# Kernel tuning notes

Measured on AMD Instinct MI355X. Metric: run time of the kernel, lower is better.

## Reference

```python
import jax, jax.numpy as jnp
import numpy as np

D_MODEL = 1024


def setup_inputs() -> dict:
    key = jax.random.key(0)
    k_x, k_qkv, k_proj, k_b = jax.random.split(key, 4)
    b, t, d = 4, 2048, D_MODEL
    scale = 1.0 / np.sqrt(d)
    x = jax.random.normal(k_x, (b, t, d), dtype=jnp.float32)
    # torch Linear(d, 3d, bias=False): weight [3d, d]; we store transposed [d, 3d]
    w_qkv = jax.random.normal(k_qkv, (d, 3 * d), dtype=jnp.float32) * scale
    w_proj = jax.random.normal(k_proj, (d, d), dtype=jnp.float32) * scale
    b_proj = jax.random.normal(k_b, (d,), dtype=jnp.float32) * scale
    return {"x": x, "w_qkv": w_qkv, "w_proj": w_proj, "b_proj": b_proj}


def reference(x, w_qkv, w_proj, b_proj):
    b, t, d = x.shape
    qkv = jnp.einsum("btd,de->bte", x, w_qkv)  # [b, t, 3d]
    q, k, v = jnp.split(qkv, 3, axis=-1)
    att = jnp.einsum("btd,bsd->bts", q, k) / jnp.sqrt(jnp.float32(d))  # [b, t, t]
    causal = jnp.tril(jnp.ones((t, t), dtype=bool))
    att = jnp.where(causal, att, -jnp.inf)
    att = jax.nn.softmax(att, axis=-1)
    out = jnp.einsum("bts,bsd->btd", att, v)
    return jnp.einsum("btd,de->bte", out, w_proj) + b_proj
```

## Files before the change

kernel.cpp:

```cpp
#include <hip/hip_runtime.h>


typedef __bf16 bf16x8_t __attribute__((ext_vector_type(8)));
typedef float  f32x4_t  __attribute__((ext_vector_type(4)));
typedef unsigned short u16;

struct alignas(8) u16x4 { u16 x, y, z, w; };

__device__ inline u16 f2bf(float f) {
  union { float f; unsigned u; } c; c.f = f;
  unsigned r = c.u + 0x7fffu + ((c.u >> 16) & 1u);
  return (u16)(r >> 16);
}

template<int OUTMODE, int GRIDMODE>
__global__ __launch_bounds__(256, 4)
void gemm_bt(const u16* __restrict__ A, const u16* __restrict__ B,
             const u16* __restrict__ B2,
             void* __restrict__ Cv, u16* __restrict__ C2,
             const float* __restrict__ bias,
             int K, int lda, int ldb, int ldc,
             long sA, long sB, long sC)
{
  int bn0, bm0;
  if (GRIDMODE == 1) {
    const int x = blockIdx.x;
    int r = (int)((sqrtf(8.f * x + 1.f) - 1.f) * 0.5f);
    while ((r + 1) * (r + 2) / 2 <= x) ++r;
    while (r * (r + 1) / 2 > x) --r;
    bm0 = r * 128;
    bn0 = (x - r * (r + 1) / 2) * 128;
  } else if (GRIDMODE == 2) {
    bn0 = blockIdx.x * 128;
    const int gy = (int)gridDim.y;
    const int yy = (blockIdx.z & 2) ? (int)blockIdx.y : (gy - 1 - (int)blockIdx.y);
    bm0 = yy * 128;
  } else {
    bn0 = blockIdx.x * 128;
    bm0 = blockIdx.y * 128;
  }
  const long bz = blockIdx.z;
  const u16* Ab = A + bz * sA;
  const u16* Bb = ((OUTMODE == 2 && bn0 >= 1024) ? B2 : B) + bz * sB;
  const int effbn = (OUTMODE == 2) ? (bn0 & 1023) : bn0;
  const int Keff = (GRIDMODE == 2) ? min(K, bm0 + 128) : K;

  __shared__ __align__(16) u16 lA[2 * 128 * 32];
  __shared__ __align__(16) u16 lB[2 * 128 * 32];

  const int tid  = threadIdx.x;
  const int lane = tid & 63;
  const int wv   = tid >> 6;
  const int wm   = (wv >> 1) << 6;
  const int wn   = (wv & 1) << 6;
  const int l15  = lane & 15;
  const int rd_off = l15 * 64 + ((((lane >> 4) ^ (l15 >> 1)) & 3) << 4);

  f32x4_t acc[4][4];
#pragma unroll
  for (int i = 0; i < 4; ++i)
#pragma unroll
    for (int j = 0; j < 4; ++j)
      acc[i][j] = (f32x4_t){0.f, 0.f, 0.f, 0.f};

  float rsacc = 0.f;

  const long ldA2 = (long)lda * 2, ldB2 = (long)ldb * 2;
  const int c_src = (tid & 3) ^ ((tid >> 3) & 3);
  const char* pA = (const char*)(Ab + (long)bm0 * lda) + (long)(tid >> 2) * ldA2 + (c_src << 4);
  const char* pB = (const char*)(Bb + (long)effbn * ldb) + (long)(tid >> 2) * ldB2 + (c_src << 4);
  const int ldsbo = tid * 16;

  for (int k0 = 0; k0 < Keff; k0 += 64) {
    const long kb = (long)k0 * 2;
#pragma unroll
    for (int r = 0; r < 4; ++r) {
      const long go = (long)(r & 1) * 64 * ldA2 + (r >> 1) * 64;
      __builtin_amdgcn_global_load_lds(
          (const __attribute__((address_space(1))) unsigned int*)(pA + kb + go),
          (__attribute__((address_space(3))) unsigned int*)((char*)lA + ldsbo + r * 4096), 16, 0, 0);
    }
#pragma unroll
    for (int r = 0; r < 4; ++r) {
      const long go = (long)(r & 1) * 64 * ldB2 + (r >> 1) * 64;
      __builtin_amdgcn_global_load_lds(
          (const __attribute__((address_space(1))) unsigned int*)(pB + kb + go),
          (__attribute__((address_space(3))) unsigned int*)((char*)lB + ldsbo + r * 4096), 16, 0, 0);
    }
    __syncthreads();

    const char* lAb = (const char*)lA + wm * 64 + rd_off;
    const char* lBb = (const char*)lB + wn * 64 + rd_off;
#pragma unroll
    for (int s = 0; s < 2; ++s) {
      const int so = s * 8192;
      bf16x8_t b0 = *(const bf16x8_t*)(lBb + so + 0 * 1024);
      bf16x8_t b1 = *(const bf16x8_t*)(lBb + so + 1 * 1024);
      bf16x8_t b2 = *(const bf16x8_t*)(lBb + so + 2 * 1024);
      bf16x8_t b3 = *(const bf16x8_t*)(lBb + so + 3 * 1024);
#pragma unroll
      for (int mf = 0; mf < 4; ++mf) {
        bf16x8_t a = *(const bf16x8_t*)(lAb + so + mf * 1024);
        acc[mf][0] = __builtin_amdgcn_mfma_f32_16x16x32_bf16(a, b0, acc[mf][0], 0, 0, 0);
        acc[mf][1] = __builtin_amdgcn_mfma_f32_16x16x32_bf16(a, b1, acc[mf][1], 0, 0, 0);
        acc[mf][2] = __builtin_amdgcn_mfma_f32_16x16x32_bf16(a, b2, acc[mf][2], 0, 0, 0);
        acc[mf][3] = __builtin_amdgcn_mfma_f32_16x16x32_bf16(a, b3, acc[mf][3], 0, 0, 0);
      }
    }

    if (OUTMODE == 4) {
      const int rr = tid >> 1;
      const int bsel = (tid & 1) * 8192;
#pragma unroll
      for (int c = 0; c < 4; ++c) {
        const int cc = (c + (rr >> 1)) & 3;
        bf16x8_t v = *(const bf16x8_t*)((const char*)lA + bsel + rr * 64 + cc * 16);
#pragma unroll
        for (int e = 0; e < 8; ++e) rsacc += (float)v[e];
      }
    }
    __syncthreads();
  }

  const int r4 = (lane >> 4) << 2;

  if (OUTMODE == 2) {
    if (bn0 >= 1024) {
#pragma unroll
      for (int mf = 0; mf < 4; ++mf) {
        const int s0 = bm0 + wm + mf * 16 + r4;
        const int b_ = s0 >> 11;
        const int s_ = s0 & 2047;
#pragma unroll
        for (int nf = 0; nf < 4; ++nf) {
          const int ocol = bn0 - 1024 + wn + nf * 16 + l15;
          u16x4 o = {f2bf(acc[mf][nf][0]), f2bf(acc[mf][nf][1]),
                     f2bf(acc[mf][nf][2]), f2bf(acc[mf][nf][3])};
          *(u16x4*)&C2[(((long)b_ * 1024 + ocol) << 11) + s_] = o;
        }
      }
    } else {
      u16* Cb16 = (u16*)Cv;
#pragma unroll
      for (int mf = 0; mf < 4; ++mf)
#pragma unroll
        for (int nf = 0; nf < 4; ++nf) {
          const int col = bn0 + wn + nf * 16 + l15;
#pragma unroll
          for (int r = 0; r < 4; ++r)
            Cb16[(long)(bm0 + wm + mf * 16 + r4 + r) * ldc + col] = f2bf(acc[mf][nf][r]);
        }
    }
    return;
  }

  if (OUTMODE == 3) {
    const float scale = 0.03125f;
    const bool diag = (bm0 == bn0);
    u16* Cb16 = (u16*)Cv + bz * sC;
#pragma unroll
    for (int mf = 0; mf < 4; ++mf)
#pragma unroll
      for (int r = 0; r < 4; ++r) {
        const int grow = bm0 + wm + mf * 16 + r4 + r;
#pragma unroll
        for (int nf = 0; nf < 4; ++nf) {
          const int col = bn0 + wn + nf * 16 + l15;
          float e = (diag && col > grow) ? 0.f : __expf(acc[mf][nf][r] * scale);
          Cb16[(long)grow * ldc + col] = f2bf(e);
        }
      }
    return;
  }

  if (OUTMODE == 4) {
    float* rsl = (float*)lA;
    rsl[tid] = rsacc;
    __syncthreads();
    float* rinv = (float*)lB;
    if (tid < 128) rinv[tid] = 1.0f / (rsl[2 * tid] + rsl[2 * tid + 1]);
    __syncthreads();
    float* Yf = (float*)Cv + bz * sC;
#pragma unroll
    for (int mf = 0; mf < 4; ++mf)
#pragma unroll
      for (int nf = 0; nf < 4; ++nf) {
        const int col = bn0 + wn + nf * 16 + l15;
        const float bb = bias[col];
#pragma unroll
        for (int r = 0; r < 4; ++r) {
          const int rl = wm + mf * 16 + r4 + r;
          Yf[(long)(bm0 + rl) * ldc + col] = acc[mf][nf][r] * rinv[rl] + bb;
        }
      }
    return;
  }
}

__global__ __launch_bounds__(256, 4)
void gemm_w(const u16* __restrict__ wfull, const u16* __restrict__ wprojT,
            u16* __restrict__ WqkT, u16* __restrict__ W2vT)
{
  const bool g2 = blockIdx.y >= 8;
  const int bm0 = ((int)blockIdx.y & 7) * 128;
  const int bn0 = (int)blockIdx.x * 128;
  const u16* A = g2 ? wprojT : (wfull + 1024);
  const u16* B = g2 ? (wfull + 2048) : wfull;
  const int lda = g2 ? 1024 : 3072;
  const int ldb = 3072;
  u16* C = g2 ? W2vT : WqkT;

  __shared__ __align__(16) u16 lA[2 * 128 * 32];
  __shared__ __align__(16) u16 lB[2 * 128 * 32];

  const int tid  = threadIdx.x;
  const int lane = tid & 63;
  const int wv   = tid >> 6;
  const int wm   = (wv >> 1) << 6;
  const int wn   = (wv & 1) << 6;
  const int l15  = lane & 15;
  const int rd_off = l15 * 64 + ((((lane >> 4) ^ (l15 >> 1)) & 3) << 4);

  f32x4_t acc[4][4];
#pragma unroll
  for (int i = 0; i < 4; ++i)
#pragma unroll
    for (int j = 0; j < 4; ++j)
      acc[i][j] = (f32x4_t){0.f, 0.f, 0.f, 0.f};

  const long ldA2 = (long)lda * 2, ldB2 = (long)ldb * 2;
  const int c_src = (tid & 3) ^ ((tid >> 3) & 3);
  const char* pA = (const char*)(A + (long)bm0 * lda) + (long)(tid >> 2) * ldA2 + (c_src << 4);
  const char* pB = (const char*)(B + (long)bn0 * ldb) + (long)(tid >> 2) * ldB2 + (c_src << 4);
  const int ldsbo = tid * 16;

  for (int k0 = 0; k0 < 1024; k0 += 64) {
    const long kb = (long)k0 * 2;
#pragma unroll
    for (int r = 0; r < 4; ++r) {
      const long go = (long)(r & 1) * 64 * ldA2 + (r >> 1) * 64;
      __builtin_amdgcn_global_load_lds(
          (const __attribute__((address_space(1))) unsigned int*)(pA + kb + go),
          (__attribute__((address_space(3))) unsigned int*)((char*)lA + ldsbo + r * 4096), 16, 0, 0);
    }
#pragma unroll
    for (int r = 0; r < 4; ++r) {
      const long go = (long)(r & 1) * 64 * ldB2 + (r >> 1) * 64;
      __builtin_amdgcn_global_load_lds(
          (const __attribute__((address_space(1))) unsigned int*)(pB + kb + go),
          (__attribute__((address_space(3))) unsigned int*)((char*)lB + ldsbo + r * 4096), 16, 0, 0);
    }
    __syncthreads();

    const char* lAb = (const char*)lA + wm * 64 + rd_off;
    const char* lBb = (const char*)lB + wn * 64 + rd_off;
#pragma unroll
    for (int s = 0; s < 2; ++s) {
      const int so = s * 8192;
      bf16x8_t b0 = *(const bf16x8_t*)(lBb + so + 0 * 1024);
      bf16x8_t b1 = *(const bf16x8_t*)(lBb + so + 1 * 1024);
      bf16x8_t b2 = *(const bf16x8_t*)(lBb + so + 2 * 1024);
      bf16x8_t b3 = *(const bf16x8_t*)(lBb + so + 3 * 1024);
#pragma unroll
      for (int mf = 0; mf < 4; ++mf) {
        bf16x8_t a = *(const bf16x8_t*)(lAb + so + mf * 1024);
        acc[mf][0] = __builtin_amdgcn_mfma_f32_16x16x32_bf16(a, b0, acc[mf][0], 0, 0, 0);
        acc[mf][1] = __builtin_amdgcn_mfma_f32_16x16x32_bf16(a, b1, acc[mf][1], 0, 0, 0);
        acc[mf][2] = __builtin_amdgcn_mfma_f32_16x16x32_bf16(a, b2, acc[mf][2], 0, 0, 0);
        acc[mf][3] = __builtin_amdgcn_mfma_f32_16x16x32_bf16(a, b3, acc[mf][3], 0, 0, 0);
      }
    }
    __syncthreads();
  }

  const int r4 = (lane >> 4) << 2;
#pragma unroll
  for (int mf = 0; mf < 4; ++mf)
#pragma unroll
    for (int nf = 0; nf < 4; ++nf) {
      const int col = bn0 + wn + nf * 16 + l15;
#pragma unroll
      for (int r = 0; r < 4; ++r)
        C[(long)(bm0 + wm + mf * 16 + r4 + r) * 1024 + col] = f2bf(acc[mf][nf][r]);
    }
}

__global__ __launch_bounds__(256)
void prep(const float* __restrict__ x, u16* __restrict__ xbf,
          const float* __restrict__ wqkv, u16* __restrict__ wfull,
          const float* __restrict__ wproj, u16* __restrict__ wprojT) {
  const int bid = blockIdx.x;
  if (bid < 8192) {
    const int i = bid * 256 + threadIdx.x;
    float4 v = ((const float4*)x)[i];
    u16x4 o = {f2bf(v.x), f2bf(v.y), f2bf(v.z), f2bf(v.w)};
    ((u16x4*)xbf)[i] = o;
    return;
  }
  if (bid < 9216) {
    const int tb = bid - 8192;
    const int c0 = (tb & 31) * 32;
    const int r0 = (tb >> 5) * 32;
    __shared__ float t[32][33];
    const int tx = threadIdx.x & 31, ty = threadIdx.x >> 5;
#pragma unroll
    for (int i = 0; i < 32; i += 8)
      t[ty + i][tx] = wproj[(long)(r0 + ty + i) * 1024 + (c0 + tx)];
    __syncthreads();
#pragma unroll
    for (int i = 0; i < 32; i += 8)
      wprojT[(long)(c0 + ty + i) * 1024 + (r0 + tx)] = f2bf(t[tx][ty + i]);
    return;
  }
  const int i = (bid - 9216) * 256 + threadIdx.x;
  float4 v = ((const float4*)wqkv)[i];
  u16x4 o = {f2bf(v.x), f2bf(v.y), f2bf(v.z), f2bf(v.w)};
  ((u16x4*)wfull)[i] = o;
}

extern "C" void kernel_launch(void* const* d_in, const int* in_sizes, int n_in,
                              void* d_out, int out_size, void* d_ws, size_t ws_size,
                              hipStream_t stream) {
  (void)in_sizes; (void)n_in; (void)out_size; (void)ws_size;
  const float* x      = (const float*)d_in[0];
  const float* w_qkv  = (const float*)d_in[1];
  const float* w_proj = (const float*)d_in[2];
  const float* b_proj = (const float*)d_in[3];
  float* y = (float*)d_out;
  char*  ws = (char*)d_ws;

  u16* xbf    = (u16*)(ws);
  u16* t1     = (u16*)(ws + (16l << 20));
  u16* WqkT   = (u16*)(ws + (32l << 20));
  u16* W2vT   = (u16*)(ws + (34l << 20));
  u16* wprojT = (u16*)(ws + (36l << 20));
  u16* wfull  = (u16*)(ws + (38l << 20));
  u16* VWT    = (u16*)(ws + (44l << 20));
  u16* E      = (u16*)(ws + (60l << 20));

  prep<<<12288, 256, 0, stream>>>(x, xbf, w_qkv, wfull, w_proj, wprojT);
  gemm_w<<<dim3(8, 16), 256, 0, stream>>>(wfull, wprojT, WqkT, W2vT);
  gemm_bt<2, 0><<<dim3(16, 64, 1), 256, 0, stream>>>(
      xbf, WqkT, W2vT, t1, VWT, nullptr, 1024, 1024, 1024, 1024, 0, 0, 0);
  gemm_bt<3, 1><<<dim3(136, 1, 4), 256, 0, stream>>>(
      t1, xbf, nullptr, E, nullptr, nullptr, 1024, 1024, 1024, 2048,
      (long)2048 * 1024, (long)2048 * 1024, (long)2048 * 2048);
  gemm_bt<4, 2><<<dim3(8, 16, 4), 256, 0, stream>>>(
      E, VWT, nullptr, y, nullptr, b_proj, 2048, 2048, 2048, 1024,
      (long)2048 * 2048, (long)1024 * 2048, (long)2048 * 1024);
}
```

Measured before the change: 238.3 us.

## Restructure launch schedule to merge independent GEMMs and prep into fewer kernels

Reorganizes the five-launch pipeline into four by regrouping independent work. Fp32-to-bf16 conversion is merged with the Wq·Wk^T weight GEMM, which converts fp32 weights inline while loading them. The x·WqkT GEMM is co-launched with the wproj·Wv GEMM, and the causal score GEMM with the x·W2v GEMM. The aim is to cut launch gaps and fill underutilized grids with independent blocks. The cost is extra branching, and the inline-converting GEMM uses slower synchronous global loads.

```diff
diff --git a/kernel.cpp b/kernel.cpp
--- a/kernel.cpp
+++ b/kernel.cpp
@@ -4,6 +4,7 @@
 typedef __bf16 bf16x8_t __attribute__((ext_vector_type(8)));
 typedef float  f32x4_t  __attribute__((ext_vector_type(4)));
 typedef unsigned short u16;
+typedef unsigned short u16x8_t __attribute__((ext_vector_type(8)));
 
 struct alignas(8) u16x4 { u16 x, y, z, w; };
 
@@ -23,14 +24,7 @@
              long sA, long sB, long sC)
 {
   int bn0, bm0;
-  if (GRIDMODE == 1) {
-    const int x = blockIdx.x;
-    int r = (int)((sqrtf(8.f * x + 1.f) - 1.f) * 0.5f);
-    while ((r + 1) * (r + 2) / 2 <= x) ++r;
-    while (r * (r + 1) / 2 > x) --r;
-    bm0 = r * 128;
-    bn0 = (x - r * (r + 1) / 2) * 128;
-  } else if (GRIDMODE == 2) {
+  if (GRIDMODE == 2) {
     bn0 = blockIdx.x * 128;
     const int gy = (int)gridDim.y;
     const int yy = (blockIdx.z & 2) ? (int)blockIdx.y : (gy - 1 - (int)blockIdx.y);
@@ -41,8 +35,7 @@
   }
   const long bz = blockIdx.z;
   const u16* Ab = A + bz * sA;
-  const u16* Bb = ((OUTMODE == 2 && bn0 >= 1024) ? B2 : B) + bz * sB;
-  const int effbn = (OUTMODE == 2) ? (bn0 & 1023) : bn0;
+  const u16* Bb = B + bz * sB;
   const int Keff = (GRIDMODE == 2) ? min(K, bm0 + 128) : K;
 
   __shared__ __align__(16) u16 lA[2 * 128 * 32];
@@ -68,7 +61,7 @@
   const long ldA2 = (long)lda * 2, ldB2 = (long)ldb * 2;
   const int c_src = (tid & 3) ^ ((tid >> 3) & 3);
   const char* pA = (const char*)(Ab + (long)bm0 * lda) + (long)(tid >> 2) * ldA2 + (c_src << 4);
-  const char* pB = (const char*)(Bb + (long)effbn * ldb) + (long)(tid >> 2) * ldB2 + (c_src << 4);
+  const char* pB = (const char*)(Bb + (long)bn0 * ldb) + (long)(tid >> 2) * ldB2 + (c_src << 4);
   const int ldsbo = tid * 16;
 
   for (int k0 = 0; k0 < Keff; k0 += 64) {
@@ -124,55 +117,6 @@
 
   const int r4 = (lane >> 4) << 2;
 
-  if (OUTMODE == 2) {
-    if (bn0 >= 1024) {
-#pragma unroll
-      for (int mf = 0; mf < 4; ++mf) {
-        const int s0 = bm0 + wm + mf * 16 + r4;
-        const int b_ = s0 >> 11;
-        const int s_ = s0 & 2047;
-#pragma unroll
-        for (int nf = 0; nf < 4; ++nf) {
-          const int ocol = bn0 - 1024 + wn + nf * 16 + l15;
-          u16x4 o = {f2bf(acc[mf][nf][0]), f2bf(acc[mf][nf][1]),
-                     f2bf(acc[mf][nf][2]), f2bf(acc[mf][nf][3])};
-          *(u16x4*)&C2[(((long)b_ * 1024 + ocol) << 11) + s_] = o;
-        }
-      }
-    } else {
-      u16* Cb16 = (u16*)Cv;
-#pragma unroll
-      for (int mf = 0; mf < 4; ++mf)
-#pragma unroll
-        for (int nf = 0; nf < 4; ++nf) {
-          const int col = bn0 + wn + nf * 16 + l15;
-#pragma unroll
-          for (int r = 0; r < 4; ++r)
-            Cb16[(long)(bm0 + wm + mf * 16 + r4 + r) * ldc + col] = f2bf(acc[mf][nf][r]);
-        }
-    }
-    return;
-  }
-
-  if (OUTMODE == 3) {
-    const float scale = 0.03125f;
-    const bool diag = (bm0 == bn0);
-    u16* Cb16 = (u16*)Cv + bz * sC;
-#pragma unroll
-    for (int mf = 0; mf < 4; ++mf)
-#pragma unroll
-      for (int r = 0; r < 4; ++r) {
-        const int grow = bm0 + wm + mf * 16 + r4 + r;
-#pragma unroll
-        for (int nf = 0; nf < 4; ++nf) {
-          const int col = bn0 + wn + nf * 16 + l15;
-          float e = (diag && col > grow) ? 0.f : __expf(acc[mf][nf][r] * scale);
-          Cb16[(long)grow * ldc + col] = f2bf(e);
-        }
-      }
-    return;
-  }
-
   if (OUTMODE == 4) {
     float* rsl = (float*)lA;
     rsl[tid] = rsacc;
@@ -195,20 +139,132 @@
       }
     return;
   }
+  (void)B2; (void)C2;
 }
 
 __global__ __launch_bounds__(256, 4)
-void gemm_w(const u16* __restrict__ wfull, const u16* __restrict__ wprojT,
-            u16* __restrict__ WqkT, u16* __restrict__ W2vT)
+void head(const float* __restrict__ x, const float* __restrict__ wqkv,
+          const float* __restrict__ wproj,
+          u16* __restrict__ xbf, u16* __restrict__ wfull,
+          u16* __restrict__ wprojT, u16* __restrict__ WqkT)
 {
-  const bool g2 = blockIdx.y >= 8;
-  const int bm0 = ((int)blockIdx.y & 7) * 128;
-  const int bn0 = (int)blockIdx.x * 128;
-  const u16* A = g2 ? wprojT : (wfull + 1024);
-  const u16* B = g2 ? (wfull + 2048) : wfull;
-  const int lda = g2 ? 1024 : 3072;
-  const int ldb = 3072;
-  u16* C = g2 ? W2vT : WqkT;
+  __shared__ __align__(16) u16 lA[2 * 128 * 32];
+  __shared__ __align__(16) u16 lB[2 * 128 * 32];
+  const int bid = blockIdx.x;
+  const int tid = threadIdx.x;
+
+  if (bid >= 64) {
+    const int cb = bid - 64;
+    if (cb < 8192) {
+      const int i = cb * 256 + tid;
+      float4 v = ((const float4*)x)[i];
+      u16x4 o = {f2bf(v.x), f2bf(v.y), f2bf(v.z), f2bf(v.w)};
+      ((u16x4*)xbf)[i] = o;
+      return;
+    }
+    if (cb < 11264) {
+      const int i = (cb - 8192) * 256 + tid;
+      float4 v = ((const float4*)wqkv)[i];
+      u16x4 o = {f2bf(v.x), f2bf(v.y), f2bf(v.z), f2bf(v.w)};
+      ((u16x4*)wfull)[i] = o;
+      return;
+    }
+    const int tb = cb - 11264;
+    const int c0 = (tb & 31) * 32;
+    const int r0 = (tb >> 5) * 32;
+    __shared__ float t[32][33];
+    const int tx = tid & 31, ty = tid >> 5;
+#pragma unroll
+    for (int i = 0; i < 32; i += 8)
+      t[ty + i][tx] = wproj[(long)(r0 + ty + i) * 1024 + (c0 + tx)];
+    __syncthreads();
+#pragma unroll
+    for (int i = 0; i < 32; i += 8)
+      wprojT[(long)(c0 + ty + i) * 1024 + (r0 + tx)] = f2bf(t[tx][ty + i]);
+    return;
+  }
+
+  const int bm0 = (bid >> 3) * 128, bn0 = (bid & 7) * 128;
+  const int lane = tid & 63;
+  const int wv   = tid >> 6;
+  const int wm   = (wv >> 1) << 6;
+  const int wn   = (wv & 1) << 6;
+  const int l15  = lane & 15;
+  const int rd_off = l15 * 64 + ((((lane >> 4) ^ (l15 >> 1)) & 3) << 4);
+  const int c_src = (tid & 3) ^ ((tid >> 3) & 3);
+  const int rowA = tid >> 2;
+
+  f32x4_t acc[4][4];
+#pragma unroll
+  for (int i = 0; i < 4; ++i)
+#pragma unroll
+    for (int j = 0; j < 4; ++j)
+      acc[i][j] = (f32x4_t){0.f, 0.f, 0.f, 0.f};
+
+  for (int k0 = 0; k0 < 1024; k0 += 64) {
+#pragma unroll
+    for (int r = 0; r < 4; ++r) {
+      const int row = rowA + (r & 1) * 64;
+      const int klog = k0 + (r >> 1) * 32 + c_src * 8;
+      const float* pa = wqkv + (long)(bm0 + row) * 3072 + 1024 + klog;
+      float4 a0 = *(const float4*)pa, a1 = *(const float4*)(pa + 4);
+      u16x8_t av = {f2bf(a0.x), f2bf(a0.y), f2bf(a0.z), f2bf(a0.w),
+                    f2bf(a1.x), f2bf(a1.y), f2bf(a1.z), f2bf(a1.w)};
+      *(u16x8_t*)((char*)lA + tid * 16 + r * 4096) = av;
+      const float* pb = wqkv + (long)(bn0 + row) * 3072 + klog;
+      float4 b0v = *(const float4*)pb, b1v = *(const float4*)(pb + 4);
+      u16x8_t bv = {f2bf(b0v.x), f2bf(b0v.y), f2bf(b0v.z), f2bf(b0v.w),
+                    f2bf(b1v.x), f2bf(b1v.y), f2bf(b1v.z), f2bf(b1v.w)};
+      *(u16x8_t*)((char*)lB + tid * 16 + r * 4096) = bv;
+    }
+    __syncthreads();
+
+    const char* lAb = (const char*)lA + wm * 64 + rd_off;
+    const char* lBb = (const char*)lB + wn * 64 + rd_off;
+#pragma unroll
+    for (int s = 0; s < 2; ++s) {
+      const int so = s * 8192;
+      bf16x8_t b0 = *(const bf16x8_t*)(lBb + so + 0 * 1024);
+      bf16x8_t b1 = *(const bf16x8_t*)(lBb + so + 1 * 1024);
+      bf16x8_t b2 = *(const bf16x8_t*)(lBb + so + 2 * 1024);
+      bf16x8_t b3 = *(const bf16x8_t*)(lBb + so + 3 * 1024);
+#pragma unroll
+      for (int mf = 0; mf < 4; ++mf) {
+        bf16x8_t a = *(const bf16x8_t*)(lAb + so + mf * 1024);
+        acc[mf][0] = __builtin_amdgcn_mfma_f32_16x16x32_bf16(a, b0, acc[mf][0], 0, 0, 0);
+        acc[mf][1] = __builtin_amdgcn_mfma_f32_16x16x32_bf16(a, b1, acc[mf][1], 0, 0, 0);
+        acc[mf][2] = __builtin_amdgcn_mfma_f32_16x16x32_bf16(a, b2, acc[mf][2], 0, 0, 0);
+        acc[mf][3] = __builtin_amdgcn_mfma_f32_16x16x32_bf16(a, b3, acc[mf][3], 0, 0, 0);
+      }
+    }
+    __syncthreads();
+  }
+
+  const int r4 = (lane >> 4) << 2;
+#pragma unroll
+  for (int mf = 0; mf < 4; ++mf)
+#pragma unroll
+    for (int nf = 0; nf < 4; ++nf) {
+      const int col = bn0 + wn + nf * 16 + l15;
+#pragma unroll
+      for (int r = 0; r < 4; ++r)
+        WqkT[(long)(bm0 + wm + mf * 16 + r4 + r) * 1024 + col] = f2bf(acc[mf][nf][r]);
+    }
+}
+
+__global__ __launch_bounds__(256, 4)
+void mix2(const u16* __restrict__ xbf, const u16* __restrict__ WqkT,
+          const u16* __restrict__ wprojT, const u16* __restrict__ wfull,
+          u16* __restrict__ t1, u16* __restrict__ W2vT)
+{
+  const int xb = blockIdx.x, yb = blockIdx.y;
+  const bool g2 = yb >= 64;
+  const int bm0 = (g2 ? (yb - 64) : yb) * 128;
+  const int bn0 = xb * 128;
+  const u16* Ab = g2 ? wprojT : xbf;
+  const u16* Bb = g2 ? (wfull + 2048) : WqkT;
+  const int ldb = g2 ? 3072 : 1024;
+  u16* C = g2 ? W2vT : t1;
 
   __shared__ __align__(16) u16 lA[2 * 128 * 32];
   __shared__ __align__(16) u16 lB[2 * 128 * 32];
@@ -228,10 +284,10 @@
     for (int j = 0; j < 4; ++j)
       acc[i][j] = (f32x4_t){0.f, 0.f, 0.f, 0.f};
 
-  const long ldA2 = (long)lda * 2, ldB2 = (long)ldb * 2;
+  const long ldA2 = 1024 * 2, ldB2 = (long)ldb * 2;
   const int c_src = (tid & 3) ^ ((tid >> 3) & 3);
-  const char* pA = (const char*)(A + (long)bm0 * lda) + (long)(tid >> 2) * ldA2 + (c_src << 4);
-  const char* pB = (const char*)(B + (long)bn0 * ldb) + (long)(tid >> 2) * ldB2 + (c_src << 4);
+  const char* pA = (const char*)(Ab + (long)bm0 * 1024) + (long)(tid >> 2) * ldA2 + (c_src << 4);
+  const char* pB = (const char*)(Bb + (long)bn0 * ldb) + (long)(tid >> 2) * ldB2 + (c_src << 4);
   const int ldsbo = tid * 16;
 
   for (int k0 = 0; k0 < 1024; k0 += 64) {
@@ -285,37 +341,131 @@
     }
 }
 
-__global__ __launch_bounds__(256)
-void prep(const float* __restrict__ x, u16* __restrict__ xbf,
-          const float* __restrict__ wqkv, u16* __restrict__ wfull,
-          const float* __restrict__ wproj, u16* __restrict__ wprojT) {
+__global__ __launch_bounds__(256, 4)
+void mix3(const u16* __restrict__ t1, const u16* __restrict__ xbf,
+          const u16* __restrict__ W2vT, u16* __restrict__ E,
+          u16* __restrict__ VWT)
+{
   const int bid = blockIdx.x;
-  if (bid < 8192) {
-    const int i = bid * 256 + threadIdx.x;
-    float4 v = ((const float4*)x)[i];
-    u16x4 o = {f2bf(v.x), f2bf(v.y), f2bf(v.z), f2bf(v.w)};
-    ((u16x4*)xbf)[i] = o;
+  const bool isS = bid < 544;
+  int bm0, bn0;
+  long z = 0;
+  const u16 *Ab, *Bb;
+  if (isS) {
+    z = bid / 136;
+    const int x = bid - (int)z * 136;
+    int r = (int)((sqrtf(8.f * x + 1.f) - 1.f) * 0.5f);
+    while ((r + 1) * (r + 2) / 2 <= x) ++r;
+    while (r * (r + 1) / 2 > x) --r;
+    bm0 = r * 128;
+    bn0 = (x - r * (r + 1) / 2) * 128;
+    Ab = t1 + z * (2048l * 1024);
+    Bb = xbf + z * (2048l * 1024);
+  } else {
+    const int i = bid - 544;
+    bm0 = (i >> 3) * 128;
+    bn0 = (i & 7) * 128;
+    Ab = xbf;
+    Bb = W2vT;
+  }
+
+  __shared__ __align__(16) u16 lA[2 * 128 * 32];
+  __shared__ __align__(16) u16 lB[2 * 128 * 32];
+
+  const int tid  = threadIdx.x;
+  const int lane = tid & 63;
+  const int wv   = tid >> 6;
+  const int wm   = (wv >> 1) << 6;
+  const int wn   = (wv & 1) << 6;
+  const int l15  = lane & 15;
+  const int rd_off = l15 * 64 + ((((lane >> 4) ^ (l15 >> 1)) & 3) << 4);
+
+  f32x4_t acc[4][4];
+#pragma unroll
+  for (int i = 0; i < 4; ++i)
+#pragma unroll
+    for (int j = 0; j < 4; ++j)
+      acc[i][j] = (f32x4_t){0.f, 0.f, 0.f, 0.f};
+
+  const long ld2 = 1024 * 2;
+  const int c_src = (tid & 3) ^ ((tid >> 3) & 3);
+  const char* pA = (const char*)(Ab + (long)bm0 * 1024) + (long)(tid >> 2) * ld2 + (c_src << 4);
+  const char* pB = (const char*)(Bb + (long)bn0 * 1024) + (long)(tid >> 2) * ld2 + (c_src << 4);
+  const int ldsbo = tid * 16;
+
+  for (int k0 = 0; k0 < 1024; k0 += 64) {
+    const long kb = (long)k0 * 2;
+#pragma unroll
+    for (int r = 0; r < 4; ++r) {
+      const long go = (long)(r & 1) * 64 * ld2 + (r >> 1) * 64;
+      __builtin_amdgcn_global_load_lds(
+          (const __attribute__((address_space(1))) unsigned int*)(pA + kb + go),
+          (__attribute__((address_space(3))) unsigned int*)((char*)lA + ldsbo + r * 4096), 16, 0, 0);
+    }
+#pragma unroll
+    for (int r = 0; r < 4; ++r) {
+      const long go = (long)(r & 1) * 64 * ld2 + (r >> 1) * 64;
+      __builtin_amdgcn_global_load_lds(
+          (const __attribute__((address_space(1))) unsigned int*)(pB + kb + go),
+          (__attribute__((address_space(3))) unsigned int*)((char*)lB + ldsbo + r * 4096), 16, 0, 0);
+    }
+    __syncthreads();
+
+    const char* lAb = (const char*)lA + wm * 64 + rd_off;
+    const char* lBb = (const char*)lB + wn * 64 + rd_off;
+#pragma unroll
+    for (int s = 0; s < 2; ++s) {
+      const int so = s * 8192;
+      bf16x8_t b0 = *(const bf16x8_t*)(lBb + so + 0 * 1024);
+      bf16x8_t b1 = *(const bf16x8_t*)(lBb + so + 1 * 1024);
+      bf16x8_t b2 = *(const bf16x8_t*)(lBb + so + 2 * 1024);
+      bf16x8_t b3 = *(const bf16x8_t*)(lBb + so + 3 * 1024);
+#pragma unroll
+      for (int mf = 0; mf < 4; ++mf) {
+        bf16x8_t a = *(const bf16x8_t*)(lAb + so + mf * 1024);
+        acc[mf][0] = __builtin_amdgcn_mfma_f32_16x16x32_bf16(a, b0, acc[mf][0], 0, 0, 0);
+        acc[mf][1] = __builtin_amdgcn_mfma_f32_16x16x32_bf16(a, b1, acc[mf][1], 0, 0, 0);
+        acc[mf][2] = __builtin_amdgcn_mfma_f32_16x16x32_bf16(a, b2, acc[mf][2], 0, 0, 0);
+        acc[mf][3] = __builtin_amdgcn_mfma_f32_16x16x32_bf16(a, b3, acc[mf][3], 0, 0, 0);
+      }
+    }
+    __syncthreads();
+  }
+
+  const int r4 = (lane >> 4) << 2;
+
+  if (isS) {
+    const float scale = 0.03125f;
+    const bool diag = (bm0 == bn0);
+    u16* Cb16 = E + z * (2048l * 2048);
+#pragma unroll
+    for (int mf = 0; mf < 4; ++mf)
+#pragma unroll
+      for (int r = 0; r < 4; ++r) {
+        const int grow = bm0 + wm + mf * 16 + r4 + r;
+#pragma unroll
+        for (int nf = 0; nf < 4; ++nf) {
+          const int col = bn0 + wn + nf * 16 + l15;
+          float e = (diag && col > grow) ? 0.f : __expf(acc[mf][nf][r] * scale);
+          Cb16[(long)grow * 2048 + col] = f2bf(e);
+        }
+      }
     return;
   }
-  if (bid < 9216) {
-    const int tb = bid - 8192;
-    const int c0 = (tb & 31) * 32;
-    const int r0 = (tb >> 5) * 32;
-    __shared__ float t[32][33];
-    const int tx = threadIdx.x & 31, ty = threadIdx.x >> 5;
-#pragma unroll
-    for (int i = 0; i < 32; i += 8)
-      t[ty + i][tx] = wproj[(long)(r0 + ty + i) * 1024 + (c0 + tx)];
-    __syncthreads();
-#pragma unroll
-    for (int i = 0; i < 32; i += 8)
-      wprojT[(long)(c0 + ty + i) * 1024 + (r0 + tx)] = f2bf(t[tx][ty + i]);
-    return;
-  }
-  const int i = (bid - 9216) * 256 + threadIdx.x;
-  float4 v = ((const float4*)wqkv)[i];
-  u16x4 o = {f2bf(v.x), f2bf(v.y), f2bf(v.z), f2bf(v.w)};
-  ((u16x4*)wfull)[i] = o;
+
+#pragma unroll
+  for (int mf = 0; mf < 4; ++mf) {
+    const int s0 = bm0 + wm + mf * 16 + r4;
+    const int b_ = s0 >> 11;
+    const int s_ = s0 & 2047;
+#pragma unroll
+    for (int nf = 0; nf < 4; ++nf) {
+      const int ocol = bn0 + wn + nf * 16 + l15;
+      u16x4 o = {f2bf(acc[mf][nf][0]), f2bf(acc[mf][nf][1]),
+                 f2bf(acc[mf][nf][2]), f2bf(acc[mf][nf][3])};
+      *(u16x4*)&VWT[(((long)b_ * 1024 + ocol) << 11) + s_] = o;
+    }
+  }
 }
 
 extern "C" void kernel_launch(void* const* d_in, const int* in_sizes, int n_in,
@@ -338,13 +488,9 @@
   u16* VWT    = (u16*)(ws + (44l << 20));
   u16* E      = (u16*)(ws + (60l << 20));
 
-  prep<<<12288, 256, 0, stream>>>(x, xbf, w_qkv, wfull, w_proj, wprojT);
-  gemm_w<<<dim3(8, 16), 256, 0, stream>>>(wfull, wprojT, WqkT, W2vT);
-  gemm_bt<2, 0><<<dim3(16, 64, 1), 256, 0, stream>>>(
-      xbf, WqkT, W2vT, t1, VWT, nullptr, 1024, 1024, 1024, 1024, 0, 0, 0);
-  gemm_bt<3, 1><<<dim3(136, 1, 4), 256, 0, stream>>>(
-      t1, xbf, nullptr, E, nullptr, nullptr, 1024, 1024, 1024, 2048,
-      (long)2048 * 1024, (long)2048 * 1024, (long)2048 * 2048);
+  head<<<12352, 256, 0, stream>>>(x, w_qkv, w_proj, xbf, wfull, wprojT, WqkT);
+  mix2<<<dim3(8, 72), 256, 0, stream>>>(xbf, WqkT, wprojT, wfull, t1, W2vT);
+  mix3<<<1056, 256, 0, stream>>>(t1, xbf, W2vT, E, VWT);
   gemm_bt<4, 2><<<dim3(8, 16, 4), 256, 0, stream>>>(
       E, VWT, nullptr, y, nullptr, b_proj, 2048, 2048, 2048, 1024,
       (long)2048 * 2048, (long)1024 * 2048, (long)2048 * 1024);
```

After: 278.8 us. 1.17x slower.

## Split final causal PV GEMM into dedicated 64-row tile kernel

Applied to the files above, without the earlier changes.

Replaces the 128x128-tile OUTMODE 4 path of the generic GEMM with a dedicated kernel that uses 64x128 tiles, with each wave owning a 32-column strip. The kernel keeps the causal K truncation, the row-sum normalisation and the bias epilogue. Halving the row tile doubles the block count (1024 blocks) and truncates the causal K range at a finer granularity, which is meant to reduce wasted work and load imbalance on the triangular E·VW product. In exchange, B tiles get less reuse, since each VWT tile is reloaded for twice as many row blocks, and per-block MFMA density is lower.

```diff
diff --git a/kernel.cpp b/kernel.cpp
--- a/kernel.cpp
+++ b/kernel.cpp
@@ -30,11 +30,6 @@
     while (r * (r + 1) / 2 > x) --r;
     bm0 = r * 128;
     bn0 = (x - r * (r + 1) / 2) * 128;
-  } else if (GRIDMODE == 2) {
-    bn0 = blockIdx.x * 128;
-    const int gy = (int)gridDim.y;
-    const int yy = (blockIdx.z & 2) ? (int)blockIdx.y : (gy - 1 - (int)blockIdx.y);
-    bm0 = yy * 128;
   } else {
     bn0 = blockIdx.x * 128;
     bm0 = blockIdx.y * 128;
@@ -43,7 +38,7 @@
   const u16* Ab = A + bz * sA;
   const u16* Bb = ((OUTMODE == 2 && bn0 >= 1024) ? B2 : B) + bz * sB;
   const int effbn = (OUTMODE == 2) ? (bn0 & 1023) : bn0;
-  const int Keff = (GRIDMODE == 2) ? min(K, bm0 + 128) : K;
+  const int Keff = K;
 
   __shared__ __align__(16) u16 lA[2 * 128 * 32];
   __shared__ __align__(16) u16 lB[2 * 128 * 32];
@@ -63,8 +58,6 @@
     for (int j = 0; j < 4; ++j)
       acc[i][j] = (f32x4_t){0.f, 0.f, 0.f, 0.f};
 
-  float rsacc = 0.f;
-
   const long ldA2 = (long)lda * 2, ldB2 = (long)ldb * 2;
   const int c_src = (tid & 3) ^ ((tid >> 3) & 3);
   const char* pA = (const char*)(Ab + (long)bm0 * lda) + (long)(tid >> 2) * ldA2 + (c_src << 4);
@@ -107,18 +100,6 @@
         acc[mf][3] = __builtin_amdgcn_mfma_f32_16x16x32_bf16(a, b3, acc[mf][3], 0, 0, 0);
       }
     }
-
-    if (OUTMODE == 4) {
-      const int rr = tid >> 1;
-      const int bsel = (tid & 1) * 8192;
-#pragma unroll
-      for (int c = 0; c < 4; ++c) {
-        const int cc = (c + (rr >> 1)) & 3;
-        bf16x8_t v = *(const bf16x8_t*)((const char*)lA + bsel + rr * 64 + cc * 16);
-#pragma unroll
-        for (int e = 0; e < 8; ++e) rsacc += (float)v[e];
-      }
-    }
     __syncthreads();
   }
 
@@ -172,29 +153,112 @@
       }
     return;
   }
-
-  if (OUTMODE == 4) {
-    float* rsl = (float*)lA;
-    rsl[tid] = rsacc;
-    __syncthreads();
-    float* rinv = (float*)lB;
-    if (tid < 128) rinv[tid] = 1.0f / (rsl[2 * tid] + rsl[2 * tid + 1]);
-    __syncthreads();
-    float* Yf = (float*)Cv + bz * sC;
-#pragma unroll
-    for (int mf = 0; mf < 4; ++mf)
-#pragma unroll
-      for (int nf = 0; nf < 4; ++nf) {
-        const int col = bn0 + wn + nf * 16 + l15;
-        const float bb = bias[col];
-#pragma unroll
-        for (int r = 0; r < 4; ++r) {
-          const int rl = wm + mf * 16 + r4 + r;
-          Yf[(long)(bm0 + rl) * ldc + col] = acc[mf][nf][r] * rinv[rl] + bb;
-        }
-      }
-    return;
-  }
+}
+
+__global__ __launch_bounds__(256, 4)
+void pv64(const u16* __restrict__ E, const u16* __restrict__ VWT,
+          float* __restrict__ Y, const float* __restrict__ bias)
+{
+  const int bn0 = blockIdx.x * 128;
+  const int yy  = (blockIdx.z & 2) ? (int)blockIdx.y : (31 - (int)blockIdx.y);
+  const int bm0 = yy * 64;
+  const long bz = blockIdx.z;
+  const u16* Ab = E + bz * (2048l * 2048);
+  const u16* Bb = VWT + bz * (1024l * 2048);
+  const int Keff = bm0 + 64;
+
+  __shared__ __align__(16) u16 lA[2 * 64 * 32];
+  __shared__ __align__(16) u16 lB[2 * 128 * 32];
+
+  const int tid  = threadIdx.x;
+  const int lane = tid & 63;
+  const int wv   = tid >> 6;
+  const int wcol = wv * 32;
+  const int l15  = lane & 15;
+  const int rd_off = l15 * 64 + ((((lane >> 4) ^ (l15 >> 1)) & 3) << 4);
+
+  f32x4_t acc[4][2];
+#pragma unroll
+  for (int i = 0; i < 4; ++i)
+#pragma unroll
+    for (int j = 0; j < 2; ++j)
+      acc[i][j] = (f32x4_t){0.f, 0.f, 0.f, 0.f};
+
+  float rsacc = 0.f;
+
+  const long ld2 = 2048 * 2;
+  const int c_src = (tid & 3) ^ ((tid >> 3) & 3);
+  const char* pA = (const char*)(Ab + (long)bm0 * 2048) + (long)(tid >> 2) * ld2 + (c_src << 4);
+  const char* pB = (const char*)(Bb + (long)bn0 * 2048) + (long)(tid >> 2) * ld2 + (c_src << 4);
+  const int ldsbo = tid * 16;
+
+  const int rs_rr  = tid >> 2;
+  const int rs_off = ((tid & 1) << 12) + rs_rr * 64 + (((tid >> 1) & 1) << 6);
+  const int rs_byte = ((tid & 1) << 12) + rs_rr * 64 + (((tid >> 1) & 1) << 5);
+
+  for (int k0 = 0; k0 < Keff; k0 += 64) {
+    const long kb = (long)k0 * 2;
+#pragma unroll
+    for (int r = 0; r < 2; ++r)
+      __builtin_amdgcn_global_load_lds(
+          (const __attribute__((address_space(1))) unsigned int*)(pA + kb + r * 64),
+          (__attribute__((address_space(3))) unsigned int*)((char*)lA + ldsbo + r * 4096), 16, 0, 0);
+#pragma unroll
+    for (int r = 0; r < 4; ++r) {
+      const long go = (long)(r & 1) * 64 * ld2 + (r >> 1) * 64;
+      __builtin_amdgcn_global_load_lds(
+          (const __attribute__((address_space(1))) unsigned int*)(pB + kb + go),
+          (__attribute__((address_space(3))) unsigned int*)((char*)lB + ldsbo + r * 4096), 16, 0, 0);
+    }
+    __syncthreads();
+
+    const char* lAb = (const char*)lA + rd_off;
+    const char* lBb = (const char*)lB + wcol * 64 + rd_off;
+#pragma unroll
+    for (int s = 0; s < 2; ++s) {
+      const int soA = s * 4096, soB = s * 8192;
+      bf16x8_t b0 = *(const bf16x8_t*)(lBb + soB + 0 * 1024);
+      bf16x8_t b1 = *(const bf16x8_t*)(lBb + soB + 1 * 1024);
+#pragma unroll
+      for (int mf = 0; mf < 4; ++mf) {
+        bf16x8_t a = *(const bf16x8_t*)(lAb + soA + mf * 1024);
+        acc[mf][0] = __builtin_amdgcn_mfma_f32_16x16x32_bf16(a, b0, acc[mf][0], 0, 0, 0);
+        acc[mf][1] = __builtin_amdgcn_mfma_f32_16x16x32_bf16(a, b1, acc[mf][1], 0, 0, 0);
+      }
+    }
+
+    {
+      bf16x8_t v0 = *(const bf16x8_t*)((const char*)lA + rs_byte);
+      bf16x8_t v1 = *(const bf16x8_t*)((const char*)lA + rs_byte + 16);
+#pragma unroll
+      for (int e = 0; e < 8; ++e) rsacc += (float)v0[e] + (float)v1[e];
+    }
+    __syncthreads();
+  }
+
+  float* rsl = (float*)lA;
+  rsl[tid] = rsacc;
+  __syncthreads();
+  float* rinv = (float*)lB;
+  if (tid < 64)
+    rinv[tid] = 1.0f / (rsl[4 * tid] + rsl[4 * tid + 1] + rsl[4 * tid + 2] + rsl[4 * tid + 3]);
+  __syncthreads();
+
+  const int r4 = (lane >> 4) << 2;
+  float* Yb = Y + bz * (2048l * 1024);
+#pragma unroll
+  for (int mf = 0; mf < 4; ++mf)
+#pragma unroll
+    for (int nf = 0; nf < 2; ++nf) {
+      const int col = bn0 + wcol + nf * 16 + l15;
+      const float bb = bias[col];
+#pragma unroll
+      for (int r = 0; r < 4; ++r) {
+        const int rl = mf * 16 + r4 + r;
+        Yb[(long)(bm0 + rl) * 1024 + col] = acc[mf][nf][r] * rinv[rl] + bb;
+      }
+    }
+  (void)rs_off;
 }
 
 __global__ __launch_bounds__(256, 4)
@@ -345,7 +409,5 @@
   gemm_bt<3, 1><<<dim3(136, 1, 4), 256, 0, stream>>>(
       t1, xbf, nullptr, E, nullptr, nullptr, 1024, 1024, 1024, 2048,
       (long)2048 * 1024, (long)2048 * 1024, (long)2048 * 2048);
-  gemm_bt<4, 2><<<dim3(8, 16, 4), 256, 0, stream>>>(
-      E, VWT, nullptr, y, nullptr, b_proj, 2048, 2048, 2048, 1024,
-      (long)2048 * 2048, (long)1024 * 2048, (long)2048 * 1024);
-}
+  pv64<<<dim3(8, 32, 4), 256, 0, stream>>>(E, VWT, y, b_proj);
+}
```

After: 235.6 us. About the same (-1.1%).
